# Optimization experiments

Hardware: AMD Instinct MI355X
Metric: run time of the kernel (lower is better)

The kernel has to match this reference:

```python
import jax, jax.numpy as jnp
import numpy as np

C = 32
C_Z = 128
S = 256
N_SEQ = 256
LN_EPS = 1e-5


def setup_inputs() -> dict:
    key = jax.random.key(0)
    k1, k2, k3, k4 = jax.random.split(key, 4)
    m_si = jax.random.normal(k1, (S, N_SEQ, C), dtype=jnp.float32)
    ln_gamma = jnp.ones((C,), dtype=jnp.float32)
    ln_beta = jnp.zeros((C,), dtype=jnp.float32)
    # nn.Linear(c, 2c, bias=False): weight shape (2c, c)
    W_ab = jax.random.normal(k2, (2 * C, C), dtype=jnp.float32) / np.sqrt(C)
    # nn.Linear(c*c, c_z): weight (c_z, c*c), bias (c_z,)
    W_out = jax.random.normal(k3, (C_Z, C * C), dtype=jnp.float32) / np.sqrt(C * C)
    b_out = jax.random.normal(k4, (C_Z,), dtype=jnp.float32) * 0.01
    return {"m_si": m_si, "ln_gamma": ln_gamma, "ln_beta": ln_beta,
            "W_ab": W_ab, "W_out": W_out, "b_out": b_out}


def reference(m_si, ln_gamma, ln_beta, W_ab, W_out, b_out):
    # LayerNorm over channel dim c
    mu = jnp.mean(m_si, axis=-1, keepdims=True)
    var = jnp.var(m_si, axis=-1, keepdims=True)
    x = (m_si - mu) * jax.lax.rsqrt(var + LN_EPS) * ln_gamma + ln_beta
    # linear_no_bias then chunk into a, b: each (s, n_seq, c)
    ab = jnp.einsum('snc,dc->snd', x, W_ab)
    a, b = ab[..., :C], ab[..., C:]
    # mean over MSA sequences of outer products a[s,i,:] x b[s,j,:]
    # restructured as a contraction over n_seq: (i, j, c, c)
    outer = jnp.einsum('inc,jnd->ijcd', a, b) / N_SEQ
    outer = outer.reshape(S, S, C * C)  # flatten (c, c) -> c*c
    # final linear projection to c_z
    z_ij = jnp.einsum('ijk,zk->ijz', outer, W_out) + b_out
    return z_ij
```

## Files before the change

### kernel.cpp

```cpp
#include <hip/hip_runtime.h>

#define SDIM 256
#define NSEQ 256
#define CDIM 32
#define CZ 128
#define IB 8
#define JB 8

typedef __bf16 bfx8 __attribute__((ext_vector_type(8)));
typedef float fx4 __attribute__((ext_vector_type(4)));
typedef float f32x16 __attribute__((ext_vector_type(16)));
typedef unsigned int u32x4 __attribute__((ext_vector_type(4)));

__device__ __forceinline__ unsigned short f2bf(float f) {
  unsigned int u = __float_as_uint(f);
  u += 0x7fffu + ((u >> 16) & 1u);
  return (unsigned short)(u >> 16);
}

__device__ __forceinline__ unsigned int cvtpk(float lo, float hi) {
  unsigned int r;
  asm("v_cvt_pk_bf16_f32 %0, %1, %2" : "=v"(r) : "v"(lo), "v"(hi));
  return r;
}

__device__ __forceinline__ bfx8 pack8(const fx4 lo, const fx4 hi) {
  bfx8 r;
  r[0] = (__bf16)lo[0]; r[1] = (__bf16)lo[1]; r[2] = (__bf16)lo[2]; r[3] = (__bf16)lo[3];
  r[4] = (__bf16)hi[0]; r[5] = (__bf16)hi[1]; r[6] = (__bf16)hi[2]; r[7] = (__bf16)hi[3];
  return r;
}

__device__ __forceinline__ void gload16(const void* g, void* l) {
  __builtin_amdgcn_global_load_lds((const __attribute__((address_space(1))) unsigned int*)g,
                                   (__attribute__((address_space(3))) unsigned int*)l,
                                   16, 0, 0);
}


__global__ __launch_bounds__(256) void opm_prep(
    const float* __restrict__ m_si, const float* __restrict__ gamma, const float* __restrict__ beta,
    const float* __restrict__ Wab, const float* __restrict__ Wout,
    unsigned short* __restrict__ a_t, unsigned short* __restrict__ b_t,
    unsigned short* __restrict__ w2T)
{
  __shared__ __align__(16) char shbuf[8192];
  const int b = blockIdx.x;
  const int t = threadIdx.x;
  if (b < SDIM) {
    const int s = b;
    const int l = t & 63;
    const int w = t >> 6;
    const int nl = l & 15;
    const int cg = l >> 4;

    bfx8 afr[4];
#pragma unroll
    for (int dt = 0; dt < 4; ++dt) {
      const float* wr = Wab + (dt * 16 + nl) * 32 + cg * 8;
      afr[dt] = pack8(*(const fx4*)wr, *(const fx4*)(wr + 4));
    }
    const fx4 g0 = *(const fx4*)(gamma + cg * 8);
    const fx4 g1 = *(const fx4*)(gamma + cg * 8 + 4);
    const fx4 bt0 = *(const fx4*)(beta + cg * 8);
    const fx4 bt1 = *(const fx4*)(beta + cg * 8 + 4);

#pragma unroll
    for (int p = 0; p < 4; ++p) {
      const int n = p * 64 + w * 16 + nl;
      const float* xr = m_si + (s * 256 + n) * 32 + cg * 8;
      const fx4 v0 = *(const fx4*)xr;
      const fx4 v1 = *(const fx4*)(xr + 4);
      float ps  = v0[0] + v0[1] + v0[2] + v0[3] + v1[0] + v1[1] + v1[2] + v1[3];
      float ps2 = v0[0]*v0[0] + v0[1]*v0[1] + v0[2]*v0[2] + v0[3]*v0[3]
                + v1[0]*v1[0] + v1[1]*v1[1] + v1[2]*v1[2] + v1[3]*v1[3];
      ps  += __shfl_xor(ps, 16);  ps  += __shfl_xor(ps, 32);
      ps2 += __shfl_xor(ps2, 16); ps2 += __shfl_xor(ps2, 32);
      const float mu = ps * 0.03125f;
      const float var = ps2 * 0.03125f - mu * mu;
      const float inv = rsqrtf(var + 1e-5f);
      const fx4 e0 = (v0 - mu) * inv * g0 + bt0;
      const fx4 e1 = (v1 - mu) * inv * g1 + bt1;
      const bfx8 bfr = pack8(e0, e1);

      fx4 dz[4];
#pragma unroll
      for (int dt = 0; dt < 4; ++dt)
        dz[dt] = __builtin_amdgcn_mfma_f32_16x16x32_bf16(afr[dt], bfr, (fx4){0.f,0.f,0.f,0.f}, 0, 0, 0);

#pragma unroll
      for (int dt = 0; dt < 4; ++dt) {
#pragma unroll
        for (int r = 0; r < 4; ++r) {
          const int d = dt * 16 + cg * 4 + r;
          const unsigned short hv = f2bf(dz[dt][r]);
          if (d < 32) a_t[(s * 32 + d) * 256 + n] = hv;
          else        b_t[(s * 32 + (d - 32)) * 256 + n] = hv;
        }
      }
    }
  } else {
    unsigned short* lin = (unsigned short*)shbuf;
    const int blk = b - SDIM;
    const float* wsrc = Wout + blk * 4096;
#pragma unroll
    for (int jj = 0; jj < 4; ++jj) {
      const int q = t + jj * 256;
      const fx4 v = ((const fx4*)wsrc)[q];
      unsigned short* dst = lin + q * 4;
      dst[0] = f2bf(v[0]); dst[1] = f2bf(v[1]); dst[2] = f2bf(v[2]); dst[3] = f2bf(v[3]);
    }
    __syncthreads();
    const int z0 = blk * 4;
#pragma unroll
    for (int w = 0; w < 2; ++w) {
      const int id = t + w * 256;
      const int lz = id & 3;
      const int hh = (id >> 2) & 1;
      const int ks = id >> 3;
      const int z = z0 + lz;
      unsigned short vals[8];
#pragma unroll
      for (int e = 0; e < 8; ++e) {
        const int kp = ks * 16 + hh * 8 + e;
        const int c = (kp & 3) | (((kp >> 8) & 1) << 2) | (((kp >> 2) & 1) << 3) | (((kp >> 9) & 1) << 4);
        const int d = (kp >> 3) & 31;
        vals[e] = lin[lz * 1024 + c * CDIM + d];
      }
      const int dest = ((z >> 5) << 15) + (ks << 9) + (hh << 8) + ((z & 31) << 3);
      *(u32x4*)(w2T + dest) = *(const u32x4*)vals;
    }
  }
}

__global__ __launch_bounds__(512, 2) void opm_main(
    const unsigned short* __restrict__ a_t, const unsigned short* __restrict__ b_t,
    const unsigned short* __restrict__ w2T, const float* __restrict__ bout,
    float* __restrict__ out)
{
  __shared__ __align__(16) char smem[131072];
  char* o_sh = smem;

  const int tid = threadIdx.x;
  const int lane = tid & 63;
  const int wid = tid >> 6;
  const int l31 = lane & 31;
  const int h = lane >> 5;

  const int bxr = blockIdx.x;
  const int xc = bxr & 7;
  const int q7 = bxr >> 3;
  const int it = (xc & 3) * 8 + (q7 >> 4);
  const int jt = (xc >> 2) * 16 + (q7 & 15);
  const int i0 = it * IB;
  const int j0 = jt * JB;

  const int wm = wid >> 2;
  const int wn = wid & 3;
  const int wbase = wid * 1024;

  f32x16 acc00 = {}, acc01 = {}, acc10 = {}, acc11 = {};
  f32x16 acc20 = {}, acc21 = {}, acc30 = {}, acc31 = {};

  auto STAGE_A = [&](int buf, int nc) {
    const int nbase = nc * 32;
    char* A = smem + buf * 16384;
#pragma unroll
    for (int pass = 0; pass < 2; ++pass) {
      const int q = pass * 512 + tid;
      const int row = q >> 2;
      const int gs = (q & 3) ^ ((q >> 3) & 3);
      const unsigned short* src = a_t + ((i0 + (row >> 5)) * 32 + (row & 31)) * 256 + nbase + gs * 8;
      gload16(src, A + pass * 8192 + wbase);
    }
  };
  auto STAGE_B = [&](int buf, int nc) {
    const int nbase = nc * 32;
    char* B = smem + 49152 + buf * 16384;
#pragma unroll
    for (int pass = 0; pass < 2; ++pass) {
      const int q = pass * 512 + tid;
      const int row = q >> 2;
      const int gs = (q & 3) ^ ((q >> 3) & 3);
      const unsigned short* src = b_t + ((j0 + (row >> 5)) * 32 + (row & 31)) * 256 + nbase + gs * 8;
      gload16(src, B + pass * 8192 + wbase);
    }
  };

  auto HALF = [&](int buf, int ks) {
    char* A = smem + buf * 16384;
    char* B = smem + 49152 + buf * 16384;
    const int s = ks * 2 + h;
    bfx8 af0, af1, af2, af3, bf0, bf1;
    { const int r = wm * 128 +  0 + l31; af0 = *(const bfx8*)(A + r * 64 + (((s ^ (r >> 1)) & 3) << 4)); }
    { const int r = wm * 128 + 32 + l31; af1 = *(const bfx8*)(A + r * 64 + (((s ^ (r >> 1)) & 3) << 4)); }
    { const int r = wm * 128 + 64 + l31; af2 = *(const bfx8*)(A + r * 64 + (((s ^ (r >> 1)) & 3) << 4)); }
    { const int r = wm * 128 + 96 + l31; af3 = *(const bfx8*)(A + r * 64 + (((s ^ (r >> 1)) & 3) << 4)); }
    { const int r = wn * 64 + l31;       bf0 = *(const bfx8*)(B + r * 64 + (((s ^ (r >> 1)) & 3) << 4)); }
    { const int r = wn * 64 + 32 + l31;  bf1 = *(const bfx8*)(B + r * 64 + (((s ^ (r >> 1)) & 3) << 4)); }
    __builtin_amdgcn_s_setprio(1);
    acc00 = __builtin_amdgcn_mfma_f32_32x32x16_bf16(af0, bf0, acc00, 0, 0, 0);
    acc01 = __builtin_amdgcn_mfma_f32_32x32x16_bf16(af0, bf1, acc01, 0, 0, 0);
    acc10 = __builtin_amdgcn_mfma_f32_32x32x16_bf16(af1, bf0, acc10, 0, 0, 0);
    acc11 = __builtin_amdgcn_mfma_f32_32x32x16_bf16(af1, bf1, acc11, 0, 0, 0);
    acc20 = __builtin_amdgcn_mfma_f32_32x32x16_bf16(af2, bf0, acc20, 0, 0, 0);
    acc21 = __builtin_amdgcn_mfma_f32_32x32x16_bf16(af2, bf1, acc21, 0, 0, 0);
    acc30 = __builtin_amdgcn_mfma_f32_32x32x16_bf16(af3, bf0, acc30, 0, 0, 0);
    acc31 = __builtin_amdgcn_mfma_f32_32x32x16_bf16(af3, bf1, acc31, 0, 0, 0);
    __builtin_amdgcn_s_setprio(0);
  };

  STAGE_A(0, 0); STAGE_B(0, 0);
  STAGE_A(1, 1); STAGE_B(1, 1);

#pragma unroll
  for (int c = 0; c < 8; ++c) {
    const int buf = c % 3;
    if (c + 2 < 8) STAGE_A((c + 2) % 3, c + 2);
    if (c <= 5)      { asm volatile("s_waitcnt vmcnt(6)" ::: "memory"); }
    else if (c == 6) { asm volatile("s_waitcnt vmcnt(4)" ::: "memory"); }
    else             { asm volatile("s_waitcnt vmcnt(0)" ::: "memory"); }
    __builtin_amdgcn_s_barrier();
    asm volatile("" ::: "memory");
    HALF(buf, 0);
    asm volatile("s_waitcnt lgkmcnt(0)" ::: "memory");
    __builtin_amdgcn_s_barrier();
    if (c + 2 < 8) STAGE_B((c + 2) % 3, c + 2);
    asm volatile("" ::: "memory");
    HALF(buf, 1);
    asm volatile("s_waitcnt lgkmcnt(0)" ::: "memory");
    __builtin_amdgcn_s_barrier();
  }
  __syncthreads();

  {
    const f32x16 av[8] = { acc00 * 0.00390625f, acc01 * 0.00390625f,
                           acc10 * 0.00390625f, acc11 * 0.00390625f,
                           acc20 * 0.00390625f, acc21 * 0.00390625f,
                           acc30 * 0.00390625f, acc31 * 0.00390625f };
#pragma unroll
    for (int sub = 0; sub < 4; ++sub) {
#pragma unroll
      for (int ni = 0; ni < 2; ++ni) {
        const f32x16 a = av[sub * 2 + ni];
        const int p = (wm * 4 + sub) * 8 + (wn * 2 + ni);
#pragma unroll
        for (int c4 = 0; c4 < 2; ++c4) {
          const int sl = l31 + 32 * h + 64 * c4;
          u32x4 v;
          v[0] = cvtpk(a[8 * c4 + 0], a[8 * c4 + 1]);
          v[1] = cvtpk(a[8 * c4 + 2], a[8 * c4 + 3]);
          v[2] = cvtpk(a[8 * c4 + 4], a[8 * c4 + 5]);
          v[3] = cvtpk(a[8 * c4 + 6], a[8 * c4 + 7]);
          *(u32x4*)(o_sh + p * 2048 + ((sl ^ (p & 7)) << 4)) = v;
        }
      }
    }
  }
  __syncthreads();

  {
    const int ztp = wid & 1;
    const int kh = wid >> 1;
    const unsigned short* wpa = w2T + ((ztp * 2 + 0) << 15) + (h << 8) + (l31 << 3);
    const unsigned short* wpb = w2T + ((ztp * 2 + 1) << 15) + (h << 8) + (l31 << 3);
    const int p0 = l31;
    const int p1 = 32 + l31;
    const int ob0 = p0 * 2048, ox0 = p0 & 7;
    const int ob1 = p1 * 2048, ox1 = p1 & 7;
    const int ks0 = kh * 16;

    bfx8 wa[4], wb[4];
#pragma unroll
    for (int q = 0; q < 4; ++q) {
      wa[q] = *(const bfx8*)(wpa + ((ks0 + q) << 9));
      wb[q] = *(const bfx8*)(wpb + ((ks0 + q) << 9));
    }
    bfx8 oc0 = *(const bfx8*)(o_sh + ob0 + ((((ks0 << 1) + h) ^ ox0) << 4));
    bfx8 on0 = *(const bfx8*)(o_sh + ob0 + (((((ks0 + 1) << 1) + h) ^ ox0) << 4));
    bfx8 oc1 = *(const bfx8*)(o_sh + ob1 + ((((ks0 << 1) + h) ^ ox1) << 4));
    bfx8 on1 = *(const bfx8*)(o_sh + ob1 + (((((ks0 + 1) << 1) + h) ^ ox1) << 4));

    f32x16 za0 = {}, zb0 = {}, za1 = {}, zb1 = {};
#pragma unroll
    for (int st = 0; st < 16; ++st) {
      const int q = st & 3;
      __builtin_amdgcn_s_setprio(1);
      za0 = __builtin_amdgcn_mfma_f32_32x32x16_bf16(wa[q], oc0, za0, 0, 0, 0);
      zb0 = __builtin_amdgcn_mfma_f32_32x32x16_bf16(wb[q], oc0, zb0, 0, 0, 0);
      za1 = __builtin_amdgcn_mfma_f32_32x32x16_bf16(wa[q], oc1, za1, 0, 0, 0);
      zb1 = __builtin_amdgcn_mfma_f32_32x32x16_bf16(wb[q], oc1, zb1, 0, 0, 0);
      __builtin_amdgcn_s_setprio(0);
      oc0 = on0; oc1 = on1;
      if (st < 14) {
        const int sl = ((ks0 + st + 2) << 1) + h;
        on0 = *(const bfx8*)(o_sh + ob0 + ((sl ^ ox0) << 4));
        on1 = *(const bfx8*)(o_sh + ob1 + ((sl ^ ox1) << 4));
      }
      if (st < 12) {
        wa[q] = *(const bfx8*)(wpa + ((ks0 + st + 4) << 9));
        wb[q] = *(const bfx8*)(wpb + ((ks0 + st + 4) << 9));
      }
    }
    __syncthreads();

    const int slot = (kh >> 1) * 2 + ztp;
    auto PWRITE = [&](char* base) {
#pragma unroll
      for (int zs = 0; zs < 2; ++zs) {
        const f32x16& A0 = zs ? zb0 : za0;
        const f32x16& A1 = zs ? zb1 : za1;
#pragma unroll
        for (int g2 = 0; g2 < 4; ++g2) {
          fx4 v0 = { A0[4 * g2], A0[4 * g2 + 1], A0[4 * g2 + 2], A0[4 * g2 + 3] };
          fx4 v1 = { A1[4 * g2], A1[4 * g2 + 1], A1[4 * g2 + 2], A1[4 * g2 + 3] };
          *(fx4*)(base + zs * 8192 + (((g2 * 2 + h) * 64 + p0) << 4)) = v0;
          *(fx4*)(base + zs * 8192 + (((g2 * 2 + h) * 64 + p1) << 4)) = v1;
        }
      }
    };
    auto PADD = [&](const char* base) {
#pragma unroll
      for (int zs = 0; zs < 2; ++zs) {
        f32x16& A0 = zs ? zb0 : za0;
        f32x16& A1 = zs ? zb1 : za1;
#pragma unroll
        for (int g2 = 0; g2 < 4; ++g2) {
          const fx4 v0 = *(const fx4*)(base + zs * 8192 + (((g2 * 2 + h) * 64 + p0) << 4));
          const fx4 v1 = *(const fx4*)(base + zs * 8192 + (((g2 * 2 + h) * 64 + p1) << 4));
          A0[4 * g2 + 0] += v0[0]; A0[4 * g2 + 1] += v0[1];
          A0[4 * g2 + 2] += v0[2]; A0[4 * g2 + 3] += v0[3];
          A1[4 * g2 + 0] += v1[0]; A1[4 * g2 + 1] += v1[1];
          A1[4 * g2 + 2] += v1[2]; A1[4 * g2 + 3] += v1[3];
        }
      }
    };
    if (kh & 1) PWRITE(o_sh + slot * 16384);
    __syncthreads();
    if (!(kh & 1)) {
      PADD(o_sh + slot * 16384);
      if (kh == 2) PWRITE(o_sh + 65536 + ztp * 16384);
    }
    __syncthreads();
    if (kh == 0) {
      PADD(o_sh + 65536 + ztp * 16384);
      const float* bp = bout + ztp * 64;
#pragma unroll
      for (int pg = 0; pg < 2; ++pg) {
        const int p = pg * 32 + l31;
        const int i = i0 + (p >> 3), j = j0 + (p & 7);
        float* op = out + (i * SDIM + j) * CZ + ztp * 64;
#pragma unroll
        for (int zs = 0; zs < 2; ++zs) {
          const f32x16& A = zs ? (pg ? zb1 : zb0) : (pg ? za1 : za0);
#pragma unroll
          for (int g2 = 0; g2 < 4; ++g2) {
            const int zl = zs * 32 + g2 * 8 + h * 4;
            fx4 v = { A[4 * g2], A[4 * g2 + 1], A[4 * g2 + 2], A[4 * g2 + 3] };
            v += *(const fx4*)(bp + zl);
            *(fx4*)(op + zl) = v;
          }
        }
      }
    }
  }
}

extern "C" void kernel_launch(void* const* d_in, const int* in_sizes, int n_in,
                              void* d_out, int out_size, void* d_ws, size_t ws_size,
                              hipStream_t stream) {
  const float* m_si  = (const float*)d_in[0];
  const float* gamma = (const float*)d_in[1];
  const float* beta  = (const float*)d_in[2];
  const float* Wab   = (const float*)d_in[3];
  const float* Wout  = (const float*)d_in[4];
  const float* bout  = (const float*)d_in[5];
  float* out = (float*)d_out;

  char* ws = (char*)d_ws;
  unsigned short* a_t = (unsigned short*)ws;
  unsigned short* b_t = (unsigned short*)(ws + (4u << 20));
  unsigned short* w2T = (unsigned short*)(ws + (8u << 20));

  opm_prep<<<dim3(SDIM + 32), dim3(256), 0, stream>>>(m_si, gamma, beta, Wab, Wout, a_t, b_t, w2T);
  opm_main<<<dim3(1024), dim3(512), 0, stream>>>(a_t, b_t, w2T, bout, out);
}
```

Before: 73.10 us.

## Merge main-loop staging barriers and remap epilogue waves to all z-tiles per pixel group

The main contraction loop now issues both the A and B staging loads for stage c+2 at the top of each iteration and drops the mid-iteration lgkmcnt wait and barrier, so each iteration has one sync point instead of two. The W_out projection epilogue reassigns waves: each wave now covers one 32-pixel group across all four 32-wide z tiles instead of two z tiles across both pixel groups. Its loads are double-buffered into A/B register sets interleaved with the MFMAs. This cuts barrier stalls and reuses each LDS operand across four MFMAs. In exchange, register pressure and weight-load traffic per wave rise, and staging B earlier relies on the triple buffer still leaving a safe gap before buffers are overwritten.

```diff
diff --git a/kernel.cpp b/kernel.cpp
--- a/kernel.cpp
+++ b/kernel.cpp
@@ -216,17 +216,13 @@
 #pragma unroll
   for (int c = 0; c < 8; ++c) {
     const int buf = c % 3;
-    if (c + 2 < 8) STAGE_A((c + 2) % 3, c + 2);
-    if (c <= 5)      { asm volatile("s_waitcnt vmcnt(6)" ::: "memory"); }
+    if (c + 2 < 8) { STAGE_A((c + 2) % 3, c + 2); STAGE_B((c + 2) % 3, c + 2); }
+    if (c <= 5)      { asm volatile("s_waitcnt vmcnt(8)" ::: "memory"); }
     else if (c == 6) { asm volatile("s_waitcnt vmcnt(4)" ::: "memory"); }
     else             { asm volatile("s_waitcnt vmcnt(0)" ::: "memory"); }
     __builtin_amdgcn_s_barrier();
     asm volatile("" ::: "memory");
     HALF(buf, 0);
-    asm volatile("s_waitcnt lgkmcnt(0)" ::: "memory");
-    __builtin_amdgcn_s_barrier();
-    if (c + 2 < 8) STAGE_B((c + 2) % 3, c + 2);
-    asm volatile("" ::: "memory");
     HALF(buf, 1);
     asm volatile("s_waitcnt lgkmcnt(0)" ::: "memory");
     __builtin_amdgcn_s_barrier();
@@ -260,106 +256,106 @@
   __syncthreads();
 
   {
-    const int ztp = wid & 1;
-    const int kh = wid >> 1;
-    const unsigned short* wpa = w2T + ((ztp * 2 + 0) << 15) + (h << 8) + (l31 << 3);
-    const unsigned short* wpb = w2T + ((ztp * 2 + 1) << 15) + (h << 8) + (l31 << 3);
-    const int p0 = l31;
-    const int p1 = 32 + l31;
-    const int ob0 = p0 * 2048, ox0 = p0 & 7;
-    const int ob1 = p1 * 2048, ox1 = p1 & 7;
+    const int kh = wid & 3;
+    const int pg = wid >> 2;
+    const int p = pg * 32 + l31;
+    const int obase = p * 2048;
+    const int oxor = p & 7;
     const int ks0 = kh * 16;
-
-    bfx8 wa[4], wb[4];
-#pragma unroll
-    for (int q = 0; q < 4; ++q) {
-      wa[q] = *(const bfx8*)(wpa + ((ks0 + q) << 9));
-      wb[q] = *(const bfx8*)(wpb + ((ks0 + q) << 9));
-    }
-    bfx8 oc0 = *(const bfx8*)(o_sh + ob0 + ((((ks0 << 1) + h) ^ ox0) << 4));
-    bfx8 on0 = *(const bfx8*)(o_sh + ob0 + (((((ks0 + 1) << 1) + h) ^ ox0) << 4));
-    bfx8 oc1 = *(const bfx8*)(o_sh + ob1 + ((((ks0 << 1) + h) ^ ox1) << 4));
-    bfx8 on1 = *(const bfx8*)(o_sh + ob1 + (((((ks0 + 1) << 1) + h) ^ ox1) << 4));
-
-    f32x16 za0 = {}, zb0 = {}, za1 = {}, zb1 = {};
-#pragma unroll
-    for (int st = 0; st < 16; ++st) {
-      const int q = st & 3;
+    const unsigned short* wp0 = w2T + (0 << 15) + (h << 8) + (l31 << 3);
+    const unsigned short* wp1 = w2T + (1 << 15) + (h << 8) + (l31 << 3);
+    const unsigned short* wp2 = w2T + (2 << 15) + (h << 8) + (l31 << 3);
+    const unsigned short* wp3 = w2T + (3 << 15) + (h << 8) + (l31 << 3);
+
+    bfx8 a0 = *(const bfx8*)(wp0 + (ks0 << 9));
+    bfx8 a1 = *(const bfx8*)(wp1 + (ks0 << 9));
+    bfx8 a2 = *(const bfx8*)(wp2 + (ks0 << 9));
+    bfx8 a3 = *(const bfx8*)(wp3 + (ks0 << 9));
+    bfx8 b0 = *(const bfx8*)(wp0 + ((ks0 + 1) << 9));
+    bfx8 b1 = *(const bfx8*)(wp1 + ((ks0 + 1) << 9));
+    bfx8 b2 = *(const bfx8*)(wp2 + ((ks0 + 1) << 9));
+    bfx8 b3 = *(const bfx8*)(wp3 + ((ks0 + 1) << 9));
+    bfx8 oA = *(const bfx8*)(o_sh + obase + (((((ks0 + 0) << 1) + h) ^ oxor) << 4));
+    bfx8 oB = *(const bfx8*)(o_sh + obase + (((((ks0 + 1) << 1) + h) ^ oxor) << 4));
+
+    f32x16 z0 = {}, z1 = {}, z2 = {}, z3 = {};
+#pragma unroll
+    for (int itr = 0; itr < 8; ++itr) {
       __builtin_amdgcn_s_setprio(1);
-      za0 = __builtin_amdgcn_mfma_f32_32x32x16_bf16(wa[q], oc0, za0, 0, 0, 0);
-      zb0 = __builtin_amdgcn_mfma_f32_32x32x16_bf16(wb[q], oc0, zb0, 0, 0, 0);
-      za1 = __builtin_amdgcn_mfma_f32_32x32x16_bf16(wa[q], oc1, za1, 0, 0, 0);
-      zb1 = __builtin_amdgcn_mfma_f32_32x32x16_bf16(wb[q], oc1, zb1, 0, 0, 0);
+      z0 = __builtin_amdgcn_mfma_f32_32x32x16_bf16(a0, oA, z0, 0, 0, 0);
+      z1 = __builtin_amdgcn_mfma_f32_32x32x16_bf16(a1, oA, z1, 0, 0, 0);
+      z2 = __builtin_amdgcn_mfma_f32_32x32x16_bf16(a2, oA, z2, 0, 0, 0);
+      z3 = __builtin_amdgcn_mfma_f32_32x32x16_bf16(a3, oA, z3, 0, 0, 0);
       __builtin_amdgcn_s_setprio(0);
-      oc0 = on0; oc1 = on1;
-      if (st < 14) {
-        const int sl = ((ks0 + st + 2) << 1) + h;
-        on0 = *(const bfx8*)(o_sh + ob0 + ((sl ^ ox0) << 4));
-        on1 = *(const bfx8*)(o_sh + ob1 + ((sl ^ ox1) << 4));
-      }
-      if (st < 12) {
-        wa[q] = *(const bfx8*)(wpa + ((ks0 + st + 4) << 9));
-        wb[q] = *(const bfx8*)(wpb + ((ks0 + st + 4) << 9));
+      if (itr < 7) {
+        const int kn = ks0 + 2 * itr + 2;
+        a0 = *(const bfx8*)(wp0 + (kn << 9));
+        a1 = *(const bfx8*)(wp1 + (kn << 9));
+        a2 = *(const bfx8*)(wp2 + (kn << 9));
+        a3 = *(const bfx8*)(wp3 + (kn << 9));
+        oA = *(const bfx8*)(o_sh + obase + ((((kn << 1) + h) ^ oxor) << 4));
+      }
+      __builtin_amdgcn_s_setprio(1);
+      z0 = __builtin_amdgcn_mfma_f32_32x32x16_bf16(b0, oB, z0, 0, 0, 0);
+      z1 = __builtin_amdgcn_mfma_f32_32x32x16_bf16(b1, oB, z1, 0, 0, 0);
+      z2 = __builtin_amdgcn_mfma_f32_32x32x16_bf16(b2, oB, z2, 0, 0, 0);
+      z3 = __builtin_amdgcn_mfma_f32_32x32x16_bf16(b3, oB, z3, 0, 0, 0);
+      __builtin_amdgcn_s_setprio(0);
+      if (itr < 7) {
+        const int kn = ks0 + 2 * itr + 3;
+        b0 = *(const bfx8*)(wp0 + (kn << 9));
+        b1 = *(const bfx8*)(wp1 + (kn << 9));
+        b2 = *(const bfx8*)(wp2 + (kn << 9));
+        b3 = *(const bfx8*)(wp3 + (kn << 9));
+        oB = *(const bfx8*)(o_sh + obase + ((((kn << 1) + h) ^ oxor) << 4));
       }
     }
     __syncthreads();
 
-    const int slot = (kh >> 1) * 2 + ztp;
+    auto ZREF = [&](int zt) -> f32x16& { return zt == 0 ? z0 : zt == 1 ? z1 : zt == 2 ? z2 : z3; };
     auto PWRITE = [&](char* base) {
 #pragma unroll
-      for (int zs = 0; zs < 2; ++zs) {
-        const f32x16& A0 = zs ? zb0 : za0;
-        const f32x16& A1 = zs ? zb1 : za1;
+      for (int zt = 0; zt < 4; ++zt) {
+        const f32x16& A = ZREF(zt);
 #pragma unroll
         for (int g2 = 0; g2 < 4; ++g2) {
-          fx4 v0 = { A0[4 * g2], A0[4 * g2 + 1], A0[4 * g2 + 2], A0[4 * g2 + 3] };
-          fx4 v1 = { A1[4 * g2], A1[4 * g2 + 1], A1[4 * g2 + 2], A1[4 * g2 + 3] };
-          *(fx4*)(base + zs * 8192 + (((g2 * 2 + h) * 64 + p0) << 4)) = v0;
-          *(fx4*)(base + zs * 8192 + (((g2 * 2 + h) * 64 + p1) << 4)) = v1;
+          fx4 v = { A[4 * g2], A[4 * g2 + 1], A[4 * g2 + 2], A[4 * g2 + 3] };
+          *(fx4*)(base + zt * 4096 + (((g2 * 2 + h) * 32 + l31) << 4)) = v;
         }
       }
     };
     auto PADD = [&](const char* base) {
 #pragma unroll
-      for (int zs = 0; zs < 2; ++zs) {
-        f32x16& A0 = zs ? zb0 : za0;
-        f32x16& A1 = zs ? zb1 : za1;
+      for (int zt = 0; zt < 4; ++zt) {
+        f32x16& A = ZREF(zt);
 #pragma unroll
         for (int g2 = 0; g2 < 4; ++g2) {
-          const fx4 v0 = *(const fx4*)(base + zs * 8192 + (((g2 * 2 + h) * 64 + p0) << 4));
-          const fx4 v1 = *(const fx4*)(base + zs * 8192 + (((g2 * 2 + h) * 64 + p1) << 4));
-          A0[4 * g2 + 0] += v0[0]; A0[4 * g2 + 1] += v0[1];
-          A0[4 * g2 + 2] += v0[2]; A0[4 * g2 + 3] += v0[3];
-          A1[4 * g2 + 0] += v1[0]; A1[4 * g2 + 1] += v1[1];
-          A1[4 * g2 + 2] += v1[2]; A1[4 * g2 + 3] += v1[3];
+          const fx4 v = *(const fx4*)(base + zt * 4096 + (((g2 * 2 + h) * 32 + l31) << 4));
+          A[4 * g2 + 0] += v[0]; A[4 * g2 + 1] += v[1];
+          A[4 * g2 + 2] += v[2]; A[4 * g2 + 3] += v[3];
         }
       }
     };
-    if (kh & 1) PWRITE(o_sh + slot * 16384);
+    if (kh & 1) PWRITE(o_sh + (pg * 2 + (kh >> 1)) * 16384);
     __syncthreads();
     if (!(kh & 1)) {
-      PADD(o_sh + slot * 16384);
-      if (kh == 2) PWRITE(o_sh + 65536 + ztp * 16384);
+      PADD(o_sh + (pg * 2 + (kh >> 1)) * 16384);
+      if (kh == 2) PWRITE(o_sh + 65536 + pg * 16384);
     }
     __syncthreads();
     if (kh == 0) {
-      PADD(o_sh + 65536 + ztp * 16384);
-      const float* bp = bout + ztp * 64;
-#pragma unroll
-      for (int pg = 0; pg < 2; ++pg) {
-        const int p = pg * 32 + l31;
-        const int i = i0 + (p >> 3), j = j0 + (p & 7);
-        float* op = out + (i * SDIM + j) * CZ + ztp * 64;
-#pragma unroll
-        for (int zs = 0; zs < 2; ++zs) {
-          const f32x16& A = zs ? (pg ? zb1 : zb0) : (pg ? za1 : za0);
-#pragma unroll
-          for (int g2 = 0; g2 < 4; ++g2) {
-            const int zl = zs * 32 + g2 * 8 + h * 4;
-            fx4 v = { A[4 * g2], A[4 * g2 + 1], A[4 * g2 + 2], A[4 * g2 + 3] };
-            v += *(const fx4*)(bp + zl);
-            *(fx4*)(op + zl) = v;
-          }
+      PADD(o_sh + 65536 + pg * 16384);
+      const int i = i0 + (p >> 3), j = j0 + (p & 7);
+      float* op = out + (i * SDIM + j) * CZ;
+#pragma unroll
+      for (int zt = 0; zt < 4; ++zt) {
+        const f32x16& A = ZREF(zt);
+#pragma unroll
+        for (int g2 = 0; g2 < 4; ++g2) {
+          const int zl = zt * 32 + g2 * 8 + h * 4;
+          fx4 v = { A[4 * g2], A[4 * g2 + 1], A[4 * g2 + 2], A[4 * g2 + 3] };
+          v += *(const fx4*)(bout + zl);
+          *(fx4*)(op + zl) = v;
         }
       }
     }
```

New measurement: 84.87 us. 1.16x slower.
